# Kernel tuning notes

Hardware: AMD Instinct MI355X
Metric: run time of the kernel (lower is better)

The kernel has to match this reference:

```python
import jax, jax.numpy as jnp
import numpy as np

H = 16          # num_attention_heads
MAX_REL = 512   # max_relative_positions


def setup_inputs() -> dict:
    key = jax.random.key(0)
    ks = jax.random.split(key, 6)
    B, N, Hid = 4, 1024, 1024
    s = 0.02
    hidden_states = jax.random.normal(ks[0], (B, N, Hid), jnp.float32)
    attention_mask = jnp.ones((B, N, N), jnp.bool_)
    ids = jnp.arange(N, dtype=jnp.int32)
    relative_pos = (ids[:, None] - ids[None, :])[None]                      # [1,N,N]
    rel_embeddings = jax.random.normal(ks[1], (2 * MAX_REL, Hid), jnp.float32)
    in_proj_w = jax.random.normal(ks[2], (3 * Hid, Hid), jnp.float32) * s
    q_bias = jnp.zeros((Hid,), jnp.float32)
    v_bias = jnp.zeros((Hid,), jnp.float32)
    pos_proj_w = jax.random.normal(ks[3], (Hid, Hid), jnp.float32) * s
    pos_q_proj_w = jax.random.normal(ks[4], (Hid, Hid), jnp.float32) * s
    pos_q_proj_b = jnp.zeros((Hid,), jnp.float32)
    return {"hidden_states": hidden_states, "attention_mask": attention_mask,
            "relative_pos": relative_pos, "rel_embeddings": rel_embeddings,
            "in_proj_w": in_proj_w, "q_bias": q_bias, "v_bias": v_bias,
            "pos_proj_w": pos_proj_w, "pos_q_proj_w": pos_q_proj_w,
            "pos_q_proj_b": pos_q_proj_b}


def reference(hidden_states, attention_mask, relative_pos, rel_embeddings,
              in_proj_w, q_bias, v_bias, pos_proj_w, pos_q_proj_w, pos_q_proj_b):
    B, N, Hid = hidden_states.shape
    D = Hid // H
    scale_factor = 3                                  # 1 + len([c2p, p2c])
    scale = jnp.sqrt(jnp.asarray(D * scale_factor, jnp.float32))

    # fused in_proj, split to per-head q/k/v (torch view order: [B,N,H,3D])
    qkv = (hidden_states @ in_proj_w.T).reshape(B, N, H, 3 * D).transpose(0, 2, 1, 3)
    q, k, v = jnp.split(qkv, 3, axis=-1)              # each [B,H,N,D]
    q = (q + q_bias.reshape(1, H, 1, D)) / scale
    v = v + v_bias.reshape(1, H, 1, D)

    scores = jnp.einsum('bhqd,bhkd->bhqk', q, k)      # [B,H,N,N]

    # ---- disentangled c2p / p2c bias ----
    span = min(N, MAX_REL)                            # attention span (static)
    rel = rel_embeddings[MAX_REL - span: MAX_REL + span]   # [2*span, Hid]
    rp = relative_pos[:, None]                        # [1,1,N,N] int

    # content -> position
    pos_k = (rel @ pos_proj_w.T).reshape(2 * span, H, D).transpose(1, 0, 2)   # [H,2s,D]
    c2p = jnp.einsum('bhqd,hsd->bhqs', q, pos_k)                              # [B,H,N,2s]
    c2p_idx = jnp.clip(rp + span, 0, 2 * span - 1)
    c2p = jnp.take_along_axis(c2p, jnp.broadcast_to(c2p_idx, (B, H, N, N)), axis=-1)

    # position -> content (pos query scaled by same sqrt(d*scale_factor))
    pos_q = ((rel @ pos_q_proj_w.T + pos_q_proj_b)
             .reshape(2 * span, H, D).transpose(1, 0, 2)) / scale             # [H,2s,D]
    p2c = jnp.einsum('bhkd,hsd->bhks', k, pos_q)                              # [B,H,N,2s]
    p2c_idx = jnp.clip(-rp + span, 0, 2 * span - 1)
    p2c = jnp.take_along_axis(p2c, jnp.broadcast_to(p2c_idx, (B, H, N, N)), axis=-1)
    p2c = p2c.swapaxes(-1, -2)                        # transpose(-1,-2)

    scores = scores + c2p + p2c

    neg = jnp.finfo(scores.dtype).min
    scores = jnp.where(attention_mask[:, None], scores, neg)
    probs = jax.nn.softmax(scores, axis=-1)
    ctx = jnp.einsum('bhqk,bhkd->bhqd', probs, v)
    return ctx.transpose(0, 2, 1, 3).reshape(B, N, Hid)
```

## Files before the change

### kernel.cpp

```cpp
#include <hip/hip_runtime.h>
#include <hip/hip_bf16.h>
#include <stdint.h>

typedef __bf16 bf16;
typedef __bf16 bf16x8 __attribute__((ext_vector_type(8)));
typedef float  f32x4  __attribute__((ext_vector_type(4)));

#define MFMA16(A_, B_, C_) __builtin_amdgcn_mfma_f32_16x16x32_bf16((A_), (B_), (C_), 0, 0, 0)
#define GLOAD_LDS16(G_, L_) __builtin_amdgcn_global_load_lds( \
    (const __attribute__((address_space(1))) void*)(G_),      \
    (__attribute__((address_space(3))) void*)(L_), 16, 0, 0)

static constexpr float INV_SCALE = 0.07216878364870322992f;

__global__ void conv_all(const float* __restrict__ s0, const float* __restrict__ s1,
                         const float* __restrict__ s2, const float* __restrict__ s3,
                         const float* __restrict__ s4,
                         bf16* __restrict__ d0, bf16* __restrict__ d1,
                         bf16* __restrict__ d2, bf16* __restrict__ d3,
                         bf16* __restrict__ d4) {
  int i = blockIdx.x * blockDim.x + threadIdx.x;
  const float* s; bf16* d; int j;
  if      (i <  524288) { s = s0; d = d0; j = i; }
  else if (i <  917504) { s = s1; d = d1; j = i -  524288; }
  else if (i < 1048576) { s = s2; d = d2; j = i -  917504; }
  else if (i < 1179648) { s = s3; d = d3; j = i - 1048576; }
  else                  { s = s4; d = d4; j = i - 1179648; }
  const float4* p = (const float4*)s + (size_t)j * 2;
  float4 a = p[0], b = p[1];
  bf16x8 o;
  o[0] = (bf16)a.x; o[1] = (bf16)a.y; o[2] = (bf16)a.z; o[3] = (bf16)a.w;
  o[4] = (bf16)b.x; o[5] = (bf16)b.y; o[6] = (bf16)b.z; o[7] = (bf16)b.w;
  *((bf16x8*)d + j) = o;
}

template<int MODE, int KTOT>
__global__ __launch_bounds__(256)
void gemm_bt(const bf16* __restrict__ A, const bf16* __restrict__ B0,
             const bf16* __restrict__ B1,
             bf16* __restrict__ o0, bf16* __restrict__ o1, bf16* __restrict__ o2,
             const float* __restrict__ bias0, const float* __restrict__ bias1,
             float scl)
{
  __shared__ bf16 As[128 * 32];
  __shared__ bf16 Bs[128 * 32];
  const int tid = threadIdx.x;
  const int w = tid >> 6, l = tid & 63;
  const int wr = w >> 1, wc = w & 1;
  const int kg = l >> 4, li = l & 15;
  const int bm = blockIdx.x * 128, bn = blockIdx.y * 128;

  const bf16* Bp = B0;
  bf16* op = o0;
  const float* bp = bias0;
  float s = scl;
  if (MODE == 1 && blockIdx.z) { Bp = B1; op = o1; bp = bias1; s = INV_SCALE; }

  const int lrow = l >> 2;
  const int lcol = (l & 3) * 8;

  f32x4 acc[4][4] = {};

  for (int k0 = 0; k0 < KTOT; k0 += 32) {
    if (k0) __syncthreads();
    #pragma unroll
    for (int i = 0; i < 2; i++) {
      int r = w * 32 + i * 16 + lrow;
      GLOAD_LDS16(A  + (size_t)(bm + r) * KTOT + k0 + lcol, As + (w * 32 + i * 16) * 32);
      GLOAD_LDS16(Bp + (size_t)(bn + r) * KTOT + k0 + lcol, Bs + (w * 32 + i * 16) * 32);
    }
    __syncthreads();
    bf16x8 af[4], bfr[4];
    #pragma unroll
    for (int m = 0; m < 4; m++)
      af[m] = *(const bf16x8*)&As[(wr * 64 + m * 16 + li) * 32 + kg * 8];
    #pragma unroll
    for (int n = 0; n < 4; n++)
      bfr[n] = *(const bf16x8*)&Bs[(wc * 64 + n * 16 + li) * 32 + kg * 8];
    #pragma unroll
    for (int m = 0; m < 4; m++)
      #pragma unroll
      for (int n = 0; n < 4; n++)
        acc[m][n] = MFMA16(af[m], bfr[n], acc[m][n]);
  }

  #pragma unroll
  for (int m = 0; m < 4; m++) {
    #pragma unroll
    for (int n = 0; n < 4; n++) {
      #pragma unroll
      for (int r = 0; r < 4; r++) {
        int i = bm + wr * 64 + m * 16 + kg * 4 + r;
        int j = bn + wc * 64 + n * 16 + li;
        float v = acc[m][n][r];
        if (MODE == 0) {
          int b = i >> 10, nn = i & 1023;
          int h = j / 192, c = j - h * 192;
          if (c < 64) {
            v = (v + bias0[h * 64 + c]) * scl;
            o0[(size_t)((b * 16 + h) * 1024 + nn) * 64 + c] = (bf16)v;
          } else if (c < 128) {
            o1[(size_t)((b * 16 + h) * 1024 + nn) * 64 + (c - 64)] = (bf16)v;
          } else {
            v += bias1[h * 64 + (c - 128)];
            o2[(size_t)((b * 16 + h) * 64 + (c - 128)) * 1024 + nn] = (bf16)v;
          }
        } else {
          if (bp) v += bp[j];
          v *= s;
          op[(size_t)((j >> 6) * 1024 + i) * 64 + (j & 63)] = (bf16)v;
        }
      }
    }
  }
}

__global__ __launch_bounds__(256)
void attn_fused(const bf16* __restrict__ q_buf, const bf16* __restrict__ k_buf,
                const bf16* __restrict__ vt_buf, const bf16* __restrict__ posk,
                const bf16* __restrict__ posq, float* __restrict__ out)
{
  __shared__ bf16 Kt[64 * 64];
  __shared__ bf16 Vt[64 * 64];
  __shared__ bf16 ring[4][16 * 132];
  __shared__ bf16 p2c_t[64 * 130];

  const int tid = threadIdx.x, w = tid >> 6, l = tid & 63;
  const int kg = l >> 4, li = l & 15;

  const int lin = blockIdx.y * 16 + blockIdx.x;
  const int xcd = lin & 7, idx = lin >> 3;
  const int bh = ((idx >> 4) << 3) | xcd;
  const int qt = idx & 15;

  const int b = bh >> 4, h = bh & 15;
  const int q0 = qt * 64;
  const int qw = q0 + w * 16;

  const bf16* qp = q_buf + ((size_t)bh * 1024 + qw) * 64;
  const bf16* kp = k_buf + (size_t)bh * 65536;
  const bf16* vp = vt_buf + (size_t)bh * 65536;
  const bf16* pk = posk + (size_t)h * 65536;
  const bf16* pq = posq + (size_t)h * 65536;
  bf16* ringw = ring[w];
  bf16* plw = Kt + w * 1024;

  bf16x8 aq[2];
  #pragma unroll
  for (int kk = 0; kk < 2; kk++)
    aq[kk] = *(const bf16x8*)(qp + li * 64 + kk * 32 + kg * 8);

  float m_r[4], l_r[4];
  f32x4 o_acc[4] = {};
  #pragma unroll
  for (int r = 0; r < 4; r++) { m_r[r] = -3.0e38f; l_r[r] = 0.f; }

  const int J0 = qw + 528;

  auto ring_fill = [&](int lo) {
    #pragma unroll
    for (int n = 0; n < 4; n++) {
      int j = lo + 16 * n + li;
      int jc = j < 0 ? 0 : (j > 1023 ? 1023 : j);
      f32x4 c = {};
      #pragma unroll
      for (int kk = 0; kk < 2; kk++) {
        bf16x8 bp_ = *(const bf16x8*)(pk + (size_t)jc * 64 + kk * 32 + kg * 8);
        c = MFMA16(aq[kk], bp_, c);
      }
      #pragma unroll
      for (int r = 0; r < 4; r++)
        ringw[(kg * 4 + r) * 132 + ((lo + 16 * n + li) & 127)] = (bf16)c[r];
    }
  };

  ring_fill(J0 - 64);

  for (int t = 0; t < 16; t++) {
    const int k0 = t * 64;
    __syncthreads();

    {
      int srow = tid >> 3;
      int su = (tid & 7) ^ (srow & 7);
      GLOAD_LDS16(kp + (size_t)(k0 + srow) * 64 + su * 8,        Kt + (w << 9));
      GLOAD_LDS16(kp + (size_t)(k0 + 32 + srow) * 64 + su * 8,   Kt + 2048 + (w << 9));
      GLOAD_LDS16(vp + (size_t)srow * 1024 + k0 + su * 8,        Vt + (w << 9));
      GLOAD_LDS16(vp + (size_t)(32 + srow) * 1024 + k0 + su * 8, Vt + 2048 + (w << 9));
    }
    ring_fill(J0 - 64 * (t + 2));
    __syncthreads();

    f32x4 sa[4] = {};
    #pragma unroll
    for (int kk = 0; kk < 2; kk++) {
      int g = kk * 4 + kg;
      #pragma unroll
      for (int n = 0; n < 4; n++) {
        int row = 16 * n + li;
        bf16x8 kB = *(const bf16x8*)&Kt[row * 64 + ((g ^ (row & 7)) * 8)];
        sa[n] = MFMA16(aq[kk], kB, sa[n]);
      }
    }
    {
      const int i0 = q0 - k0 + 449;
      f32x4 pca[4][2] = {};
      #pragma unroll
      for (int kk = 0; kk < 2; kk++) {
        int g = kk * 4 + kg;
        bf16x8 kA[4];
        #pragma unroll
        for (int m = 0; m < 4; m++) {
          int row = 16 * m + li;
          kA[m] = *(const bf16x8*)&Kt[row * 64 + ((g ^ (row & 7)) * 8)];
        }
        #pragma unroll
        for (int n2 = 0; n2 < 2; n2++) {
          int i = i0 + 32 * w + 16 * n2 + li;
          int ic = i < 0 ? 0 : (i > 1023 ? 1023 : i);
          bf16x8 qB = *(const bf16x8*)(pq + (size_t)ic * 64 + kk * 32 + kg * 8);
          #pragma unroll
          for (int m = 0; m < 4; m++)
            pca[m][n2] = MFMA16(kA[m], qB, pca[m][n2]);
        }
      }
      #pragma unroll
      for (int m = 0; m < 4; m++)
        #pragma unroll
        for (int n2 = 0; n2 < 2; n2++)
          #pragma unroll
          for (int r = 0; r < 4; r++)
            p2c_t[(16 * m + kg * 4 + r) * 130 + 32 * w + 16 * n2 + li] = (bf16)pca[m][n2][r];
    }
    __syncthreads();

    float sv[4][4];
    #pragma unroll
    for (int n = 0; n < 4; n++) {
      #pragma unroll
      for (int r = 0; r < 4; r++) {
        int q = kg * 4 + r;
        int qg = qw + q;
        int k = k0 + 16 * n + li;
        int j = qg - k + 512;
        float cpv = (float)ringw[q * 132 + (j & 127)];
        int pcoff = (qg - q0) - (k - k0) + 63;
        float pcv = (float)p2c_t[(k - k0) * 130 + pcoff];
        sv[n][r] = sa[n][r] + cpv + pcv;
      }
    }
    #pragma unroll
    for (int r = 0; r < 4; r++) {
      float rmax = fmaxf(fmaxf(sv[0][r], sv[1][r]), fmaxf(sv[2][r], sv[3][r]));
      #pragma unroll
      for (int d = 1; d < 16; d <<= 1) rmax = fmaxf(rmax, __shfl_xor(rmax, d));
      float mnew = fmaxf(m_r[r], rmax);
      float sc = __expf(m_r[r] - mnew);
      m_r[r] = mnew;
      float rs = 0.f;
      #pragma unroll
      for (int n = 0; n < 4; n++) {
        float e = __expf(sv[n][r] - mnew);
        sv[n][r] = e;
        rs += e;
      }
      #pragma unroll
      for (int d = 1; d < 16; d <<= 1) rs += __shfl_xor(rs, d);
      l_r[r] = l_r[r] * sc + rs;
      #pragma unroll
      for (int n = 0; n < 4; n++) o_acc[n][r] *= sc;
    }
    #pragma unroll
    for (int n = 0; n < 4; n++)
      #pragma unroll
      for (int r = 0; r < 4; r++) {
        int q = kg * 4 + r;
        int k = 16 * n + li;
        plw[q * 64 + (((k >> 3) ^ (q & 7)) * 8) + (k & 7)] = (bf16)sv[n][r];
      }
    #pragma unroll
    for (int kk = 0; kk < 2; kk++) {
      int g = kk * 4 + kg;
      bf16x8 pA = *(const bf16x8*)&plw[li * 64 + ((g ^ (li & 7)) * 8)];
      #pragma unroll
      for (int n = 0; n < 4; n++) {
        int row = 16 * n + li;
        bf16x8 vB = *(const bf16x8*)&Vt[row * 64 + ((g ^ (row & 7)) * 8)];
        o_acc[n] = MFMA16(pA, vB, o_acc[n]);
      }
    }
  }

  #pragma unroll
  for (int n = 0; n < 4; n++)
    #pragma unroll
    for (int r = 0; r < 4; r++)
      out[((size_t)(b * 1024 + qw + kg * 4 + r)) * 1024 + h * 64 + 16 * n + li] =
          o_acc[n][r] / l_r[r];
}

extern "C" void kernel_launch(void* const* d_in, const int* in_sizes, int n_in,
                              void* d_out, int out_size, void* d_ws, size_t ws_size,
                              hipStream_t stream)
{
  (void)in_sizes; (void)n_in; (void)out_size;
  const float* hs   = (const float*)d_in[0];
  const float* rel  = (const float*)d_in[3];
  const float* wqkv = (const float*)d_in[4];
  const float* qb   = (const float*)d_in[5];
  const float* vb   = (const float*)d_in[6];
  const float* wpk  = (const float*)d_in[7];
  const float* wpq  = (const float*)d_in[8];
  const float* pqb  = (const float*)d_in[9];
  float* out = (float*)d_out;
  char* ws = (char*)d_ws;

  size_t off = 0;
  auto alloc = [&](size_t elems) { bf16* p = (bf16*)(ws + off); off += elems * 2; return p; };
  bf16* hs_b   = alloc((size_t)4 << 20);
  bf16* wq_b   = alloc((size_t)3 << 20);
  bf16* rel_b  = alloc((size_t)1 << 20);
  bf16* wpk_b  = alloc((size_t)1 << 20);
  bf16* wpq_b  = alloc((size_t)1 << 20);
  bf16* q_buf  = alloc((size_t)4 << 20);
  bf16* k_buf  = alloc((size_t)4 << 20);
  bf16* vt_buf = alloc((size_t)4 << 20);
  bf16* posk   = alloc((size_t)1 << 20);
  bf16* posq   = alloc((size_t)1 << 20);
  if (ws_size < off) return;

  conv_all<<<5120, 256, 0, stream>>>(hs, wqkv, rel, wpk, wpq,
                                     hs_b, wq_b, rel_b, wpk_b, wpq_b);

  gemm_bt<0, 1024><<<dim3(32, 24, 1), 256, 0, stream>>>(
      hs_b, wq_b, nullptr, q_buf, k_buf, vt_buf, qb, vb, INV_SCALE);
  gemm_bt<1, 1024><<<dim3(8, 8, 2), 256, 0, stream>>>(
      rel_b, wpk_b, wpq_b, posk, posq, nullptr, nullptr, pqb, 1.0f);

  attn_fused<<<dim3(16, 64, 1), 256, 0, stream>>>(
      q_buf, k_buf, vt_buf, posk, posq, out);
}
```

Measured before the change: 261.3 us.

## Enlarge attention query tile to 128 with 512 threads and merge projection GEMMs

Each attention block now covers 128 queries with 8 waves instead of 64 queries with 4. The per-tile K/V loads are therefore shared across twice as many queries, and the c2p ring and p2c band buffers are reorganised into shared LDS layouts that allow vectorised reads. The p2c computation is repartitioned so each wave computes six 16-column strips of a band, and the PV product is split into two 32-key halves, reusing a smaller per-wave P buffer. The two projection GEMM launches are merged into one launch with a flat block index. The trade-offs are higher LDS use per block, a larger band computation, and a launch bound of 4 that may pressure registers.

```diff
diff --git a/kernel.cpp b/kernel.cpp
--- a/kernel.cpp
+++ b/kernel.cpp
@@ -3,6 +3,8 @@
 #include <stdint.h>
 
 typedef __bf16 bf16;
+typedef __bf16 bf16x2 __attribute__((ext_vector_type(2)));
+typedef __bf16 bf16x4 __attribute__((ext_vector_type(4)));
 typedef __bf16 bf16x8 __attribute__((ext_vector_type(8)));
 typedef float  f32x4  __attribute__((ext_vector_type(4)));
 
@@ -34,13 +36,15 @@
   *((bf16x8*)d + j) = o;
 }
 
-template<int MODE, int KTOT>
 __global__ __launch_bounds__(256)
-void gemm_bt(const bf16* __restrict__ A, const bf16* __restrict__ B0,
-             const bf16* __restrict__ B1,
-             bf16* __restrict__ o0, bf16* __restrict__ o1, bf16* __restrict__ o2,
-             const float* __restrict__ bias0, const float* __restrict__ bias1,
-             float scl)
+void gemm_all(const bf16* __restrict__ hs, const bf16* __restrict__ wq,
+              const bf16* __restrict__ rel, const bf16* __restrict__ wpk,
+              const bf16* __restrict__ wpq,
+              bf16* __restrict__ q_buf, bf16* __restrict__ k_buf,
+              bf16* __restrict__ vt_buf, bf16* __restrict__ posk,
+              bf16* __restrict__ posq,
+              const float* __restrict__ qb, const float* __restrict__ vb,
+              const float* __restrict__ pqb)
 {
   __shared__ bf16 As[128 * 32];
   __shared__ bf16 Bs[128 * 32];
@@ -48,26 +52,30 @@
   const int w = tid >> 6, l = tid & 63;
   const int wr = w >> 1, wc = w & 1;
   const int kg = l >> 4, li = l & 15;
-  const int bm = blockIdx.x * 128, bn = blockIdx.y * 128;
-
-  const bf16* Bp = B0;
-  bf16* op = o0;
-  const float* bp = bias0;
-  float s = scl;
-  if (MODE == 1 && blockIdx.z) { Bp = B1; op = o1; bp = bias1; s = INV_SCALE; }
+
+  const int bid = blockIdx.x;
+  int mode, bm, bn;
+  const bf16 *A, *B;
+  if (bid < 768) { mode = 0; bm = (bid & 31) * 128; bn = (bid >> 5) * 128; A = hs; B = wq; }
+  else {
+    int pb = bid - 768;
+    mode = 1 + (pb >> 6);
+    bm = (pb & 7) * 128; bn = ((pb >> 3) & 7) * 128;
+    A = rel; B = (mode == 1) ? wpk : wpq;
+  }
 
   const int lrow = l >> 2;
   const int lcol = (l & 3) * 8;
 
   f32x4 acc[4][4] = {};
 
-  for (int k0 = 0; k0 < KTOT; k0 += 32) {
+  for (int k0 = 0; k0 < 1024; k0 += 32) {
     if (k0) __syncthreads();
     #pragma unroll
     for (int i = 0; i < 2; i++) {
       int r = w * 32 + i * 16 + lrow;
-      GLOAD_LDS16(A  + (size_t)(bm + r) * KTOT + k0 + lcol, As + (w * 32 + i * 16) * 32);
-      GLOAD_LDS16(Bp + (size_t)(bn + r) * KTOT + k0 + lcol, Bs + (w * 32 + i * 16) * 32);
+      GLOAD_LDS16(A + (size_t)(bm + r) * 1024 + k0 + lcol, As + (w * 32 + i * 16) * 32);
+      GLOAD_LDS16(B + (size_t)(bn + r) * 1024 + k0 + lcol, Bs + (w * 32 + i * 16) * 32);
     }
     __syncthreads();
     bf16x8 af[4], bfr[4];
@@ -93,21 +101,21 @@
         int i = bm + wr * 64 + m * 16 + kg * 4 + r;
         int j = bn + wc * 64 + n * 16 + li;
         float v = acc[m][n][r];
-        if (MODE == 0) {
+        if (mode == 0) {
           int b = i >> 10, nn = i & 1023;
           int h = j / 192, c = j - h * 192;
           if (c < 64) {
-            v = (v + bias0[h * 64 + c]) * scl;
-            o0[(size_t)((b * 16 + h) * 1024 + nn) * 64 + c] = (bf16)v;
+            v = (v + qb[h * 64 + c]) * INV_SCALE;
+            q_buf[(size_t)((b * 16 + h) * 1024 + nn) * 64 + c] = (bf16)v;
           } else if (c < 128) {
-            o1[(size_t)((b * 16 + h) * 1024 + nn) * 64 + (c - 64)] = (bf16)v;
+            k_buf[(size_t)((b * 16 + h) * 1024 + nn) * 64 + (c - 64)] = (bf16)v;
           } else {
-            v += bias1[h * 64 + (c - 128)];
-            o2[(size_t)((b * 16 + h) * 64 + (c - 128)) * 1024 + nn] = (bf16)v;
+            v += vb[h * 64 + (c - 128)];
+            vt_buf[(size_t)((b * 16 + h) * 64 + (c - 128)) * 1024 + nn] = (bf16)v;
           }
         } else {
-          if (bp) v += bp[j];
-          v *= s;
+          if (mode == 2) v = (v + pqb[j]) * INV_SCALE;
+          bf16* op = (mode == 1) ? posk : posq;
           op[(size_t)((j >> 6) * 1024 + i) * 64 + (j & 63)] = (bf16)v;
         }
       }
@@ -115,26 +123,26 @@
   }
 }
 
-__global__ __launch_bounds__(256)
+__global__ __launch_bounds__(512, 4)
 void attn_fused(const bf16* __restrict__ q_buf, const bf16* __restrict__ k_buf,
                 const bf16* __restrict__ vt_buf, const bf16* __restrict__ posk,
                 const bf16* __restrict__ posq, float* __restrict__ out)
 {
-  __shared__ bf16 Kt[64 * 64];
-  __shared__ bf16 Vt[64 * 64];
-  __shared__ bf16 ring[4][16 * 132];
-  __shared__ bf16 p2c_t[64 * 130];
+  __shared__ __align__(16) bf16 Kt[64 * 64];
+  __shared__ __align__(16) bf16 Vt[64 * 64];
+  __shared__ __align__(16) bf16 ring2[128 * 130];
+  __shared__ __align__(16) bf16 band[64 * 196];
 
   const int tid = threadIdx.x, w = tid >> 6, l = tid & 63;
   const int kg = l >> 4, li = l & 15;
 
-  const int lin = blockIdx.y * 16 + blockIdx.x;
+  const int lin = blockIdx.y * 8 + blockIdx.x;
   const int xcd = lin & 7, idx = lin >> 3;
-  const int bh = ((idx >> 4) << 3) | xcd;
-  const int qt = idx & 15;
+  const int bh = ((idx >> 3) << 3) | xcd;
+  const int qt = idx & 7;
 
   const int b = bh >> 4, h = bh & 15;
-  const int q0 = qt * 64;
+  const int q0 = qt * 128;
   const int qw = q0 + w * 16;
 
   const bf16* qp = q_buf + ((size_t)bh * 1024 + qw) * 64;
@@ -142,8 +150,6 @@
   const bf16* vp = vt_buf + (size_t)bh * 65536;
   const bf16* pk = posk + (size_t)h * 65536;
   const bf16* pq = posq + (size_t)h * 65536;
-  bf16* ringw = ring[w];
-  bf16* plw = Kt + w * 1024;
 
   bf16x8 aq[2];
   #pragma unroll
@@ -169,8 +175,10 @@
         c = MFMA16(aq[kk], bp_, c);
       }
       #pragma unroll
-      for (int r = 0; r < 4; r++)
-        ringw[(kg * 4 + r) * 132 + ((lo + 16 * n + li) & 127)] = (bf16)c[r];
+      for (int r = 0; r < 4; r++) {
+        int rowf = (j - (qw + kg * 4 + r)) & 127;
+        ring2[rowf * 130 + w * 16 + kg * 4 + r] = (bf16)c[r];
+      }
     }
   };
 
@@ -183,10 +191,8 @@
     {
       int srow = tid >> 3;
       int su = (tid & 7) ^ (srow & 7);
-      GLOAD_LDS16(kp + (size_t)(k0 + srow) * 64 + su * 8,        Kt + (w << 9));
-      GLOAD_LDS16(kp + (size_t)(k0 + 32 + srow) * 64 + su * 8,   Kt + 2048 + (w << 9));
-      GLOAD_LDS16(vp + (size_t)srow * 1024 + k0 + su * 8,        Vt + (w << 9));
-      GLOAD_LDS16(vp + (size_t)(32 + srow) * 1024 + k0 + su * 8, Vt + 2048 + (w << 9));
+      GLOAD_LDS16(kp + (size_t)(k0 + srow) * 64 + su * 8,  Kt + (w << 9));
+      GLOAD_LDS16(vp + (size_t)srow * 1024 + k0 + su * 8,  Vt + (w << 9));
     }
     ring_fill(J0 - 64 * (t + 2));
     __syncthreads();
@@ -204,50 +210,46 @@
     }
     {
       const int i0 = q0 - k0 + 449;
-      f32x4 pca[4][2] = {};
-      #pragma unroll
-      for (int kk = 0; kk < 2; kk++) {
-        int g = kk * 4 + kg;
-        bf16x8 kA[4];
+      const int mW = w & 3;
+      const int rowA = 16 * mW + li;
+      bf16x8 kA[2];
+      #pragma unroll
+      for (int kk = 0; kk < 2; kk++)
+        kA[kk] = *(const bf16x8*)&Kt[rowA * 64 + (((kk * 4 + kg) ^ (rowA & 7)) * 8)];
+      const int ctb = (w >> 2) * 6;
+      #pragma unroll
+      for (int c6 = 0; c6 < 6; c6++) {
+        int ct = ctb + c6;
+        int i = i0 + ct * 16 + li;
+        int ic = i < 0 ? 0 : (i > 1023 ? 1023 : i);
+        f32x4 pca = {};
         #pragma unroll
-        for (int m = 0; m < 4; m++) {
-          int row = 16 * m + li;
-          kA[m] = *(const bf16x8*)&Kt[row * 64 + ((g ^ (row & 7)) * 8)];
+        for (int kk = 0; kk < 2; kk++) {
+          bf16x8 qB = *(const bf16x8*)(pq + (size_t)ic * 64 + kk * 32 + kg * 8);
+          pca = MFMA16(kA[kk], qB, pca);
         }
+        int colc = ct * 16 + li;
         #pragma unroll
-        for (int n2 = 0; n2 < 2; n2++) {
-          int i = i0 + 32 * w + 16 * n2 + li;
-          int ic = i < 0 ? 0 : (i > 1023 ? 1023 : i);
-          bf16x8 qB = *(const bf16x8*)(pq + (size_t)ic * 64 + kk * 32 + kg * 8);
-          #pragma unroll
-          for (int m = 0; m < 4; m++)
-            pca[m][n2] = MFMA16(kA[m], qB, pca[m][n2]);
-        }
-      }
-      #pragma unroll
-      for (int m = 0; m < 4; m++)
-        #pragma unroll
-        for (int n2 = 0; n2 < 2; n2++)
-          #pragma unroll
-          for (int r = 0; r < 4; r++)
-            p2c_t[(16 * m + kg * 4 + r) * 130 + 32 * w + 16 * n2 + li] = (bf16)pca[m][n2][r];
+        for (int r = 0; r < 4; r++)
+          band[(16 * mW + kg * 4 + r) * 196 + colc + r + 1] = (bf16)pca[r];
+      }
     }
     __syncthreads();
 
     float sv[4][4];
     #pragma unroll
     for (int n = 0; n < 4; n++) {
-      #pragma unroll
-      for (int r = 0; r < 4; r++) {
-        int q = kg * 4 + r;
-        int qg = qw + q;
-        int k = k0 + 16 * n + li;
-        int j = qg - k + 512;
-        float cpv = (float)ringw[q * 132 + (j & 127)];
-        int pcoff = (qg - q0) - (k - k0) + 63;
-        float pcv = (float)p2c_t[(k - k0) * 130 + pcoff];
-        sv[n][r] = sa[n][r] + cpv + pcv;
-      }
+      int kl = 16 * n + li;
+      int rowr = (512 - (k0 + kl)) & 127;
+      const bf16* rbase = &ring2[rowr * 130 + w * 16 + kg * 4];
+      bf16x2 ra = *(const bf16x2*)rbase;
+      bf16x2 rb = *(const bf16x2*)(rbase + 2);
+      int c0s = w * 16 + kg * 4 - kl + 63 + (li & 3) + 1;
+      bf16x4 bb = *(const bf16x4*)&band[kl * 196 + c0s];
+      sv[n][0] = sa[n][0] + (float)ra[0] + (float)bb[0];
+      sv[n][1] = sa[n][1] + (float)ra[1] + (float)bb[1];
+      sv[n][2] = sa[n][2] + (float)rb[0] + (float)bb[2];
+      sv[n][3] = sa[n][3] + (float)rb[1] + (float)bb[3];
     }
     #pragma unroll
     for (int r = 0; r < 4; r++) {
@@ -270,22 +272,24 @@
       #pragma unroll
       for (int n = 0; n < 4; n++) o_acc[n][r] *= sc;
     }
-    #pragma unroll
-    for (int n = 0; n < 4; n++)
-      #pragma unroll
-      for (int r = 0; r < 4; r++) {
-        int q = kg * 4 + r;
-        int k = 16 * n + li;
-        plw[q * 64 + (((k >> 3) ^ (q & 7)) * 8) + (k & 7)] = (bf16)sv[n][r];
-      }
-    #pragma unroll
-    for (int kk = 0; kk < 2; kk++) {
-      int g = kk * 4 + kg;
-      bf16x8 pA = *(const bf16x8*)&plw[li * 64 + ((g ^ (li & 7)) * 8)];
+    bf16* plw = Kt + (w << 9);
+    #pragma unroll
+    for (int ck = 0; ck < 2; ck++) {
+      #pragma unroll
+      for (int n2 = 0; n2 < 2; n2++) {
+        #pragma unroll
+        for (int r = 0; r < 4; r++) {
+          int q = kg * 4 + r;
+          int kpr = n2 * 16 + li;
+          int phys = (kpr >> 3) ^ ((q >> 1) & 3);
+          plw[q * 32 + phys * 8 + (kpr & 7)] = (bf16)sv[ck * 2 + n2][r];
+        }
+      }
+      bf16x8 pA = *(const bf16x8*)&plw[li * 32 + ((kg ^ ((li >> 1) & 3)) * 8)];
       #pragma unroll
       for (int n = 0; n < 4; n++) {
         int row = 16 * n + li;
-        bf16x8 vB = *(const bf16x8*)&Vt[row * 64 + ((g ^ (row & 7)) * 8)];
+        bf16x8 vB = *(const bf16x8*)&Vt[row * 64 + (((ck * 4 + kg) ^ (row & 7)) * 8)];
         o_acc[n] = MFMA16(pA, vB, o_acc[n]);
       }
     }
@@ -332,11 +336,10 @@
   conv_all<<<5120, 256, 0, stream>>>(hs, wqkv, rel, wpk, wpq,
                                      hs_b, wq_b, rel_b, wpk_b, wpq_b);
 
-  gemm_bt<0, 1024><<<dim3(32, 24, 1), 256, 0, stream>>>(
-      hs_b, wq_b, nullptr, q_buf, k_buf, vt_buf, qb, vb, INV_SCALE);
-  gemm_bt<1, 1024><<<dim3(8, 8, 2), 256, 0, stream>>>(
-      rel_b, wpk_b, wpq_b, posk, posq, nullptr, nullptr, pqb, 1.0f);
-
-  attn_fused<<<dim3(16, 64, 1), 256, 0, stream>>>(
+  gemm_all<<<896, 256, 0, stream>>>(hs_b, wq_b, rel_b, wpk_b, wpq_b,
+                                    q_buf, k_buf, vt_buf, posk, posq,
+                                    qb, vb, pqb);
+
+  attn_fused<<<dim3(8, 64), 512, 0, stream>>>(
       q_buf, k_buf, vt_buf, posk, posq, out);
 }
```

New measurement: 247.4 us. -5.3%, faster.
